# Optimization experiments

Measured on AMD Instinct MI355X. Metric: run time of the kernel, lower is better.

Reference implementation:

```python
import jax, jax.numpy as jnp
import numpy as np

N_CELLS = 50000
HID = 64
DEG = 16
K_NODES = 4  # nodes per cell; cell i owns nodes [4i, 4i+4)
SP = 3


def setup_inputs() -> dict:
    key = jax.random.key(0)
    ks = jax.random.split(key, 12)
    s = 1.0 / np.sqrt(HID)
    inp = {
        'features': jax.random.normal(ks[0], (N_CELLS, HID), jnp.float32),
        'positions': jax.random.normal(ks[1], (K_NODES * N_CELLS, SP), jnp.float32),
        'neighbors': jax.random.randint(ks[2], (N_CELLS, DEG), 0, N_CELLS, jnp.int32),
        # message MLP: Linear(2H+1 -> H), SiLU, Linear(H -> H)
        'W1': jax.random.normal(ks[3], (2 * HID + 1, HID), jnp.float32) * s,
        'b1': jnp.zeros((HID,), jnp.float32),
        'W2': jax.random.normal(ks[4], (HID, HID), jnp.float32) * s,
        'b2': jnp.zeros((HID,), jnp.float32),
        # update MLP: Linear(H + H -> H), SiLU, Linear(H -> H)
        'Wu1': jax.random.normal(ks[5], (2 * HID, HID), jnp.float32) * s,
        'bu1': jnp.zeros((HID,), jnp.float32),
        'Wu2': jax.random.normal(ks[6], (HID, HID), jnp.float32) * s,
        'bu2': jnp.zeros((HID,), jnp.float32),
    }
    return inp


def reference(features, positions, neighbors, W1, b1, W2, b2, Wu1, bu1, Wu2, bu2):
    N, H = features.shape
    # centroid of each cell's owned nodes (cell i -> nodes [K*i, K*i+K))
    cent = positions.reshape(N, K_NODES, SP).mean(axis=1)          # [N, sp]
    fj = features[neighbors]                                       # [N, D, H]
    cj = cent[neighbors]                                           # [N, D, sp]
    # centroid-distance geometric invariant per (cell, neighbor) pair
    geom = jnp.linalg.norm(cent[:, None, :] - cj, axis=-1, keepdims=True)  # [N, D, 1]
    fi = jnp.broadcast_to(features[:, None, :], fj.shape)          # [N, D, H]
    x = jnp.concatenate([fi, fj, geom], axis=-1)                   # [N, D, 2H+1]
    h = jax.nn.silu(x @ W1 + b1) @ W2 + b2                         # [N, D, H]
    msg = h.mean(axis=1)                                           # mean over neighbors
    u = jnp.concatenate([features, msg], axis=-1)                  # [N, 2H]
    upd = jax.nn.silu(u @ Wu1 + bu1) @ Wu2 + bu2
    updated_features = features + upd
    return updated_features, positions
```

## Files before the change

### kernel.cpp

```cpp
#include <hip/hip_runtime.h>


#define DEG 16

typedef __attribute__((ext_vector_type(8))) short short8;
typedef __attribute__((ext_vector_type(4))) float f32x4;
typedef uint2 uint2_a __attribute__((may_alias));
typedef uint4 uint4_a __attribute__((may_alias));

union HbRd { uint4_a u; short8 s; };

__device__ __forceinline__ unsigned f2bf(float f) {
  unsigned u = __float_as_uint(f);
  return (u + 0x7FFFu + ((u >> 16) & 1u)) >> 16;
}
__device__ __forceinline__ float bf2f(unsigned bits16) {
  return __uint_as_float(bits16 << 16);
}
__device__ __forceinline__ float silu(float h) {
  return h / (1.f + __expf(-h));
}

__global__ __launch_bounds__(256) void prep_kernel(
    const float* __restrict__ feat, const float* __restrict__ pos,
    const float* __restrict__ W1, const float* __restrict__ W2,
    const float* __restrict__ Wu1, const float* __restrict__ Wu2,
    unsigned short* __restrict__ featb, float* __restrict__ cent4,
    float* __restrict__ outpos,
    unsigned short* __restrict__ w1pq, unsigned short* __restrict__ w2t,
    unsigned short* __restrict__ wu1t, unsigned short* __restrict__ wu2b)
{
  int t = blockIdx.x * 256 + threadIdx.x;
  if (t < 800000) {
    const float4 v = ((const float4*)feat)[t];
    ushort4 b;
    b.x = (unsigned short)f2bf(v.x);
    b.y = (unsigned short)f2bf(v.y);
    b.z = (unsigned short)f2bf(v.z);
    b.w = (unsigned short)f2bf(v.w);
    ((ushort4*)featb)[t] = b;
  } else if (t < 950000) {
    const int p = t - 800000;
    ((float4*)outpos)[p] = ((const float4*)pos)[p];
  } else if (t < 1000000) {
    const int i = t - 950000;
    const float4* pp = (const float4*)(pos + 12 * i);
    const float4 a = pp[0], b = pp[1], c = pp[2];
    float4 o;
    o.x = (a.x + a.w + b.z + c.y) * 0.25f;
    o.y = (a.y + b.x + b.w + c.z) * 0.25f;
    o.z = (a.z + b.y + c.x + c.w) * 0.25f;
    o.w = 0.f;
    ((float4*)cent4)[i] = o;
  } else if (t < 1024576) {
    const int r = t - 1000000;
    if (r < 8192) {
      const int j = r & 7, l = (r >> 3) & 15, q = (r >> 7) & 3;
      const int f = r >> 9, kk = f & 1, mt = f >> 1;
      const int k = kk * 32 + q * 8 + j;
      const int m = mt * 16 + l;
      w1pq[r] = (unsigned short)f2bf(
          (m < 64) ? W1[k * 64 + m] : W1[(k + 64) * 64 + (m - 64)]);
    } else if (r < 12288) {
      const int s = r - 8192;
      const int j = s & 7, l = (s >> 3) & 15, q = (s >> 7) & 3;
      const int f = s >> 9, kk = f & 1, mt = f >> 1;
      const int k = kk * 32 + q * 8 + j;
      w2t[s] = (unsigned short)f2bf(W2[k * 64 + mt * 16 + l]);
    } else if (r < 20480) {
      const int s = r - 12288;
      const int j = s & 7, l = (s >> 3) & 15, q = (s >> 7) & 3;
      const int f = s >> 9, kk = f & 3, mt = f >> 2;
      const int k = kk * 32 + q * 8 + j;
      wu1t[s] = (unsigned short)f2bf(Wu1[k * 64 + mt * 16 + l]);
    } else {
      const int s = r - 20480;
      const int j = s & 7, l = (s >> 3) & 15, q = (s >> 7) & 3;
      const int f = s >> 9, kk = f & 1, nt = f >> 1;
      const int k = kk * 32 + q * 8 + j;
      wu2b[s] = (unsigned short)f2bf(Wu2[k * 64 + nt * 16 + l]);
    }
  }
}

__global__ __launch_bounds__(256) void pq_kernel(
    const unsigned short* __restrict__ featb,
    const unsigned short* __restrict__ w1pq,
    unsigned short* __restrict__ PQ)
{
  const int lane = threadIdx.x & 63;
  const int wid  = threadIdx.x >> 6;
  const int quad = lane >> 4;
  const int l15  = lane & 15;

  short8 wf[8][2];
  #pragma unroll
  for (int mt = 0; mt < 8; ++mt)
    #pragma unroll
    for (int kk = 0; kk < 2; ++kk)
      wf[mt][kk] = *(const short8*)(w1pq + (((mt * 2 + kk) * 4 + quad) << 7) + l15 * 8);

  const int tile = blockIdx.x * 4 + wid;
  const bool act = (tile < 3125);
  const int  tt  = act ? tile : 3124;
  const int  cr  = tt * 16 + l15;

  short8 xf[2];
  #pragma unroll
  for (int kk = 0; kk < 2; ++kk)
    xf[kk] = *(const short8*)(featb + cr * 64 + kk * 32 + quad * 8);

  f32x4 acc[8] = {};
  #pragma unroll
  for (int kk = 0; kk < 2; ++kk)
    #pragma unroll
    for (int mt = 0; mt < 8; ++mt)
      acc[mt] = __builtin_amdgcn_mfma_f32_16x16x32_bf16(wf[mt][kk], xf[kk], acc[mt], 0, 0, 0);

  if (act) {
    #pragma unroll
    for (int mt = 0; mt < 8; ++mt) {
      uint2 pk;
      pk.x = f2bf(acc[mt][0]) | (f2bf(acc[mt][1]) << 16);
      pk.y = f2bf(acc[mt][2]) | (f2bf(acc[mt][3]) << 16);
      *(uint2*)(PQ + cr * 128 + mt * 16 + quad * 4) = pk;
    }
  }
}

__global__ __launch_bounds__(256) void gather_kernel(
    const unsigned short* __restrict__ PQ,
    const float4* __restrict__ cent4,
    const int* __restrict__ nbr,
    const float* __restrict__ b1, const float* __restrict__ W1,
    unsigned short* __restrict__ sB)
{
  const int lane = threadIdx.x & 63;
  const int wid  = threadIdx.x >> 6;
  const int quad = lane >> 4;
  const int l15  = lane & 15;
  const int c4   = l15 * 4;

  const f32x4 b1c = *(const f32x4*)(b1 + c4);
  const f32x4 wlc = *(const f32x4*)(W1 + 8192 + c4);

  for (int c = blockIdx.x * 4 + wid; c < 50000; c += 12500) {
    int nj = 0; float g = 0.f;
    if (lane < 16) {
      nj = nbr[c * DEG + lane];
      const float4 ci = cent4[c];
      const float4 cj = cent4[nj];
      const float dx = ci.x - cj.x, dy = ci.y - cj.y, dz = ci.z - cj.z;
      g = sqrtf(dx * dx + dy * dy + dz * dz);
    }

    const uint2 pv = *(const uint2*)(PQ + c * 128 + c4);
    float pc[4];
    pc[0] = bf2f(pv.x & 0xFFFFu) + b1c[0];
    pc[1] = bf2f(pv.x >> 16)     + b1c[1];
    pc[2] = bf2f(pv.y & 0xFFFFu) + b1c[2];
    pc[3] = bf2f(pv.y >> 16)     + b1c[3];

    float acc0 = 0.f, acc1 = 0.f, acc2 = 0.f, acc3 = 0.f;
    #pragma unroll
    for (int dd = 0; dd < 4; ++dd) {
      const int   d  = quad + dd * 4;
      const float gd = __shfl(g, d);
      const int   nd = __shfl(nj, d);
      const uint2 qv = *(const uint2*)(PQ + nd * 128 + 64 + c4);
      acc0 += silu(pc[0] + bf2f(qv.x & 0xFFFFu) + gd * wlc[0]);
      acc1 += silu(pc[1] + bf2f(qv.x >> 16)     + gd * wlc[1]);
      acc2 += silu(pc[2] + bf2f(qv.y & 0xFFFFu) + gd * wlc[2]);
      acc3 += silu(pc[3] + bf2f(qv.y >> 16)     + gd * wlc[3]);
    }
    acc0 += __shfl_xor(acc0, 16); acc0 += __shfl_xor(acc0, 32);
    acc1 += __shfl_xor(acc1, 16); acc1 += __shfl_xor(acc1, 32);
    acc2 += __shfl_xor(acc2, 16); acc2 += __shfl_xor(acc2, 32);
    acc3 += __shfl_xor(acc3, 16); acc3 += __shfl_xor(acc3, 32);

    if (lane < 16) {
      uint2 pk;
      pk.x = f2bf(acc0 * 0.0625f) | (f2bf(acc1 * 0.0625f) << 16);
      pk.y = f2bf(acc2 * 0.0625f) | (f2bf(acc3 * 0.0625f) << 16);
      *(uint2*)(sB + c * 64 + c4) = pk;
    }
  }
}

__global__ __launch_bounds__(256) void tail_kernel(
    const unsigned short* __restrict__ featb,
    const unsigned short* __restrict__ sB,
    const float* __restrict__ feat,
    const unsigned short* __restrict__ w2t,
    const unsigned short* __restrict__ wu1t,
    const unsigned short* __restrict__ wu2b,
    const float* __restrict__ b2, const float* __restrict__ bu1,
    const float* __restrict__ bu2,
    float* __restrict__ outf)
{
  __shared__ uint4 smem[4 * 288];
  const int lane = threadIdx.x & 63;
  const int wid  = threadIdx.x >> 6;
  const int quad = lane >> 4;
  const int l15  = lane & 15;
  char* Msg = (char*)(smem + wid * 288);
  char* Hb  = Msg + 2304;

  short8 w2f[4][2];
  #pragma unroll
  for (int mt = 0; mt < 4; ++mt)
    #pragma unroll
    for (int kk = 0; kk < 2; ++kk)
      w2f[mt][kk] = *(const short8*)(w2t + (((mt * 2 + kk) * 4 + quad) << 7) + l15 * 8);
  short8 wu1f[4][4];
  #pragma unroll
  for (int mt = 0; mt < 4; ++mt)
    #pragma unroll
    for (int kk = 0; kk < 4; ++kk)
      wu1f[mt][kk] = *(const short8*)(wu1t + (((mt * 4 + kk) * 4 + quad) << 7) + l15 * 8);
  short8 wu2f[4][2];
  #pragma unroll
  for (int nt = 0; nt < 4; ++nt)
    #pragma unroll
    for (int kk = 0; kk < 2; ++kk)
      wu2f[nt][kk] = *(const short8*)(wu2b + (((nt * 2 + kk) * 4 + quad) << 7) + l15 * 8);

  f32x4 b2f[4], bu1f[4];
  #pragma unroll
  for (int mt = 0; mt < 4; ++mt) {
    b2f[mt]  = *(const f32x4*)(b2  + mt * 16 + quad * 4);
    bu1f[mt] = *(const f32x4*)(bu1 + mt * 16 + quad * 4);
  }
  float bu2v[4];
  #pragma unroll
  for (int nt = 0; nt < 4; ++nt) bu2v[nt] = bu2[nt * 16 + l15];

  const int tile = blockIdx.x * 4 + wid;
  const bool act = (tile < 3125);
  const int  tt  = act ? tile : 3124;
  const int  cr  = tt * 16 + l15;

  f32x4 accm[4] = {};
  #pragma unroll
  for (int kk = 0; kk < 2; ++kk) {
    const short8 bf = *(const short8*)(sB + cr * 64 + kk * 32 + quad * 8);
    #pragma unroll
    for (int mt = 0; mt < 4; ++mt)
      accm[mt] = __builtin_amdgcn_mfma_f32_16x16x32_bf16(w2f[mt][kk], bf, accm[mt], 0, 0, 0);
  }
  #pragma unroll
  for (int mt = 0; mt < 4; ++mt) {
    uint2 pk;
    pk.x = f2bf(accm[mt][0] + b2f[mt][0]) | (f2bf(accm[mt][1] + b2f[mt][1]) << 16);
    pk.y = f2bf(accm[mt][2] + b2f[mt][2]) | (f2bf(accm[mt][3] + b2f[mt][3]) << 16);
    *(uint2_a*)(Msg + l15 * 144 + mt * 32 + quad * 8) = pk;
  }
  __threadfence_block();

  f32x4 accu[4] = {};
  #pragma unroll
  for (int kk = 0; kk < 4; ++kk) {
    short8 bf;
    if (kk < 2) {
      bf = *(const short8*)(featb + cr * 64 + kk * 32 + quad * 8);
    } else {
      HbRd t; t.u = *(const uint4_a*)(Msg + l15 * 144 + (kk - 2) * 64 + quad * 16);
      bf = t.s;
    }
    #pragma unroll
    for (int mt = 0; mt < 4; ++mt)
      accu[mt] = __builtin_amdgcn_mfma_f32_16x16x32_bf16(wu1f[mt][kk], bf, accu[mt], 0, 0, 0);
  }
  #pragma unroll
  for (int mt = 0; mt < 4; ++mt) {
    float sv[4];
    #pragma unroll
    for (int rg = 0; rg < 4; ++rg)
      sv[rg] = silu(accu[mt][rg] + bu1f[mt][rg]);
    uint2 pk;
    pk.x = f2bf(sv[0]) | (f2bf(sv[1]) << 16);
    pk.y = f2bf(sv[2]) | (f2bf(sv[3]) << 16);
    *(uint2_a*)(Hb + l15 * 144 + mt * 32 + quad * 8) = pk;
  }
  __threadfence_block();

  f32x4 acc2[4] = {};
  #pragma unroll
  for (int kk = 0; kk < 2; ++kk) {
    HbRd t; t.u = *(const uint4_a*)(Hb + l15 * 144 + kk * 64 + quad * 16);
    const short8 af = t.s;
    #pragma unroll
    for (int nt = 0; nt < 4; ++nt)
      acc2[nt] = __builtin_amdgcn_mfma_f32_16x16x32_bf16(af, wu2f[nt][kk], acc2[nt], 0, 0, 0);
  }
  if (act) {
    #pragma unroll
    for (int nt = 0; nt < 4; ++nt)
      #pragma unroll
      for (int rg = 0; rg < 4; ++rg) {
        const int row = tt * 16 + quad * 4 + rg;
        const int col = nt * 16 + l15;
        outf[row * 64 + col] = feat[row * 64 + col] + acc2[nt][rg] + bu2v[nt];
      }
  }
}

extern "C" void kernel_launch(void* const* d_in, const int* in_sizes, int n_in,
                              void* d_out, int out_size, void* d_ws, size_t ws_size,
                              hipStream_t stream)
{
  const float* feat = (const float*)d_in[0];
  const float* pos  = (const float*)d_in[1];
  const int*   nbr  = (const int*)d_in[2];
  const float* W1   = (const float*)d_in[3];
  const float* b1   = (const float*)d_in[4];
  const float* W2   = (const float*)d_in[5];
  const float* b2   = (const float*)d_in[6];
  const float* Wu1  = (const float*)d_in[7];
  const float* bu1  = (const float*)d_in[8];
  const float* Wu2  = (const float*)d_in[9];
  const float* bu2  = (const float*)d_in[10];
  float* out = (float*)d_out;

  unsigned short* featb = (unsigned short*)d_ws;
  unsigned short* PQ    = (unsigned short*)((char*)d_ws + 6400000);
  unsigned short* sB    = (unsigned short*)((char*)d_ws + 19200000);
  float*          cent4 = (float*)((char*)d_ws + 25600000);
  unsigned short* w1pq  = (unsigned short*)((char*)d_ws + 26400000);
  unsigned short* w2t   = (unsigned short*)((char*)d_ws + 26416384);
  unsigned short* wu1t  = (unsigned short*)((char*)d_ws + 26424576);
  unsigned short* wu2b  = (unsigned short*)((char*)d_ws + 26440960);

  prep_kernel<<<4003, 256, 0, stream>>>(feat, pos, W1, W2, Wu1, Wu2,
                                        featb, cent4, out + 3200000,
                                        w1pq, w2t, wu1t, wu2b);
  pq_kernel<<<782, 256, 0, stream>>>(featb, w1pq, PQ);
  gather_kernel<<<3125, 256, 0, stream>>>(PQ, (const float4*)cent4, nbr,
                                          b1, W1, sB);
  tail_kernel<<<782, 256, 0, stream>>>(featb, sB, feat, w2t, wu1t, wu2b,
                                       b2, bu1, bu2, out);
}
```

Before: 144.1 us.

## Fuse feature bf16 conversion and centroid into PQ kernel; split P/Q buffers

The fp32-to-bf16 feature conversion and the centroid computation move from the prep kernel into the PQ GEMM kernel. The GEMM now reads fp32 features directly, converts them in registers, and writes featb as a side output. This removes one full write-then-read of the bf16 feature array between kernels and shrinks the prep kernel to the position copy and weight packing. The PQ output is also split into separate P and Q arrays, so each neighbor gather for Q reads a contiguous 64-element row instead of half of a 128-wide row, which should improve locality for the random gathers. In exchange, the PQ kernel carries more loads and conversion work before its MFMAs.

```diff
diff --git a/kernel.cpp b/kernel.cpp
--- a/kernel.cpp
+++ b/kernel.cpp
@@ -9,6 +9,7 @@
 typedef uint4 uint4_a __attribute__((may_alias));
 
 union HbRd { uint4_a u; short8 s; };
+union Frag { short8 s; uint4 u; };
 
 __device__ __forceinline__ unsigned f2bf(float f) {
   unsigned u = __float_as_uint(f);
@@ -21,39 +22,19 @@
   return h / (1.f + __expf(-h));
 }
 
-__global__ __launch_bounds__(256) void prep_kernel(
-    const float* __restrict__ feat, const float* __restrict__ pos,
+__global__ __launch_bounds__(256) void aux_kernel(
+    const float* __restrict__ pos,
     const float* __restrict__ W1, const float* __restrict__ W2,
     const float* __restrict__ Wu1, const float* __restrict__ Wu2,
-    unsigned short* __restrict__ featb, float* __restrict__ cent4,
     float* __restrict__ outpos,
     unsigned short* __restrict__ w1pq, unsigned short* __restrict__ w2t,
     unsigned short* __restrict__ wu1t, unsigned short* __restrict__ wu2b)
 {
   int t = blockIdx.x * 256 + threadIdx.x;
-  if (t < 800000) {
-    const float4 v = ((const float4*)feat)[t];
-    ushort4 b;
-    b.x = (unsigned short)f2bf(v.x);
-    b.y = (unsigned short)f2bf(v.y);
-    b.z = (unsigned short)f2bf(v.z);
-    b.w = (unsigned short)f2bf(v.w);
-    ((ushort4*)featb)[t] = b;
-  } else if (t < 950000) {
-    const int p = t - 800000;
-    ((float4*)outpos)[p] = ((const float4*)pos)[p];
-  } else if (t < 1000000) {
-    const int i = t - 950000;
-    const float4* pp = (const float4*)(pos + 12 * i);
-    const float4 a = pp[0], b = pp[1], c = pp[2];
-    float4 o;
-    o.x = (a.x + a.w + b.z + c.y) * 0.25f;
-    o.y = (a.y + b.x + b.w + c.z) * 0.25f;
-    o.z = (a.z + b.y + c.x + c.w) * 0.25f;
-    o.w = 0.f;
-    ((float4*)cent4)[i] = o;
-  } else if (t < 1024576) {
-    const int r = t - 1000000;
+  if (t < 150000) {
+    ((float4*)outpos)[t] = ((const float4*)pos)[t];
+  } else if (t < 174576) {
+    const int r = t - 150000;
     if (r < 8192) {
       const int j = r & 7, l = (r >> 3) & 15, q = (r >> 7) & 3;
       const int f = r >> 9, kk = f & 1, mt = f >> 1;
@@ -83,23 +64,17 @@
   }
 }
 
-__global__ __launch_bounds__(256) void pq_kernel(
-    const unsigned short* __restrict__ featb,
+__global__ __launch_bounds__(256) void prep_pq_kernel(
+    const float* __restrict__ feat, const float* __restrict__ pos,
     const unsigned short* __restrict__ w1pq,
-    unsigned short* __restrict__ PQ)
+    unsigned short* __restrict__ featb, float* __restrict__ cent4,
+    unsigned short* __restrict__ Pb, unsigned short* __restrict__ Qb)
 {
   const int lane = threadIdx.x & 63;
   const int wid  = threadIdx.x >> 6;
   const int quad = lane >> 4;
   const int l15  = lane & 15;
 
-  short8 wf[8][2];
-  #pragma unroll
-  for (int mt = 0; mt < 8; ++mt)
-    #pragma unroll
-    for (int kk = 0; kk < 2; ++kk)
-      wf[mt][kk] = *(const short8*)(w1pq + (((mt * 2 + kk) * 4 + quad) << 7) + l15 * 8);
-
   const int tile = blockIdx.x * 4 + wid;
   const bool act = (tile < 3125);
   const int  tt  = act ? tile : 3124;
@@ -107,8 +82,35 @@
 
   short8 xf[2];
   #pragma unroll
-  for (int kk = 0; kk < 2; ++kk)
-    xf[kk] = *(const short8*)(featb + cr * 64 + kk * 32 + quad * 8);
+  for (int kk = 0; kk < 2; ++kk) {
+    const float4 f0 = *(const float4*)(feat + cr * 64 + kk * 32 + quad * 8);
+    const float4 f1 = *(const float4*)(feat + cr * 64 + kk * 32 + quad * 8 + 4);
+    Frag v;
+    v.s[0] = (short)f2bf(f0.x); v.s[1] = (short)f2bf(f0.y);
+    v.s[2] = (short)f2bf(f0.z); v.s[3] = (short)f2bf(f0.w);
+    v.s[4] = (short)f2bf(f1.x); v.s[5] = (short)f2bf(f1.y);
+    v.s[6] = (short)f2bf(f1.z); v.s[7] = (short)f2bf(f1.w);
+    xf[kk] = v.s;
+    if (act) *(uint4*)(featb + cr * 64 + kk * 32 + quad * 8) = v.u;
+  }
+
+  if (act && lane < 16) {
+    const float4* pp = (const float4*)(pos + 12 * cr);
+    const float4 a = pp[0], b = pp[1], c = pp[2];
+    float4 o;
+    o.x = (a.x + a.w + b.z + c.y) * 0.25f;
+    o.y = (a.y + b.x + b.w + c.z) * 0.25f;
+    o.z = (a.z + b.y + c.x + c.w) * 0.25f;
+    o.w = 0.f;
+    ((float4*)cent4)[cr] = o;
+  }
+
+  short8 wf[8][2];
+  #pragma unroll
+  for (int mt = 0; mt < 8; ++mt)
+    #pragma unroll
+    for (int kk = 0; kk < 2; ++kk)
+      wf[mt][kk] = *(const short8*)(w1pq + (((mt * 2 + kk) * 4 + quad) << 7) + l15 * 8);
 
   f32x4 acc[8] = {};
   #pragma unroll
@@ -123,13 +125,17 @@
       uint2 pk;
       pk.x = f2bf(acc[mt][0]) | (f2bf(acc[mt][1]) << 16);
       pk.y = f2bf(acc[mt][2]) | (f2bf(acc[mt][3]) << 16);
-      *(uint2*)(PQ + cr * 128 + mt * 16 + quad * 4) = pk;
+      unsigned short* dst = (mt < 4)
+          ? Pb + cr * 64 + mt * 16 + quad * 4
+          : Qb + cr * 64 + (mt - 4) * 16 + quad * 4;
+      *(uint2*)dst = pk;
     }
   }
 }
 
 __global__ __launch_bounds__(256) void gather_kernel(
-    const unsigned short* __restrict__ PQ,
+    const unsigned short* __restrict__ Pb,
+    const unsigned short* __restrict__ Qb,
     const float4* __restrict__ cent4,
     const int* __restrict__ nbr,
     const float* __restrict__ b1, const float* __restrict__ W1,
@@ -154,7 +160,7 @@
       g = sqrtf(dx * dx + dy * dy + dz * dz);
     }
 
-    const uint2 pv = *(const uint2*)(PQ + c * 128 + c4);
+    const uint2 pv = *(const uint2*)(Pb + c * 64 + c4);
     float pc[4];
     pc[0] = bf2f(pv.x & 0xFFFFu) + b1c[0];
     pc[1] = bf2f(pv.x >> 16)     + b1c[1];
@@ -167,7 +173,7 @@
       const int   d  = quad + dd * 4;
       const float gd = __shfl(g, d);
       const int   nd = __shfl(nj, d);
-      const uint2 qv = *(const uint2*)(PQ + nd * 128 + 64 + c4);
+      const uint2 qv = *(const uint2*)(Qb + nd * 64 + c4);
       acc0 += silu(pc[0] + bf2f(qv.x & 0xFFFFu) + gd * wlc[0]);
       acc1 += silu(pc[1] + bf2f(qv.x >> 16)     + gd * wlc[1]);
       acc2 += silu(pc[2] + bf2f(qv.y & 0xFFFFu) + gd * wlc[2]);
@@ -323,7 +329,8 @@
   float* out = (float*)d_out;
 
   unsigned short* featb = (unsigned short*)d_ws;
-  unsigned short* PQ    = (unsigned short*)((char*)d_ws + 6400000);
+  unsigned short* Pb    = (unsigned short*)((char*)d_ws + 6400000);
+  unsigned short* Qb    = (unsigned short*)((char*)d_ws + 12800000);
   unsigned short* sB    = (unsigned short*)((char*)d_ws + 19200000);
   float*          cent4 = (float*)((char*)d_ws + 25600000);
   unsigned short* w1pq  = (unsigned short*)((char*)d_ws + 26400000);
@@ -331,11 +338,10 @@
   unsigned short* wu1t  = (unsigned short*)((char*)d_ws + 26424576);
   unsigned short* wu2b  = (unsigned short*)((char*)d_ws + 26440960);
 
-  prep_kernel<<<4003, 256, 0, stream>>>(feat, pos, W1, W2, Wu1, Wu2,
-                                        featb, cent4, out + 3200000,
-                                        w1pq, w2t, wu1t, wu2b);
-  pq_kernel<<<782, 256, 0, stream>>>(featb, w1pq, PQ);
-  gather_kernel<<<3125, 256, 0, stream>>>(PQ, (const float4*)cent4, nbr,
+  aux_kernel<<<682, 256, 0, stream>>>(pos, W1, W2, Wu1, Wu2, out + 3200000,
+                                      w1pq, w2t, wu1t, wu2b);
+  prep_pq_kernel<<<782, 256, 0, stream>>>(feat, pos, w1pq, featb, cent4, Pb, Qb);
+  gather_kernel<<<3125, 256, 0, stream>>>(Pb, Qb, (const float4*)cent4, nbr,
                                           b1, W1, sB);
   tail_kernel<<<782, 256, 0, stream>>>(featb, sB, feat, w2t, wu1t, wu2b,
                                        b2, bu1, bu2, out);
```

New measurement: 143.2 us. No clear change (-0.7%).
